# Kernel optimization log

Hardware: AMD Instinct MI355X
Metric: run time of the kernel (lower is better)

Reference implementation:

```python
import jax, jax.numpy as jnp
import numpy as np

N_EMBEDS = 1024
N_HEADS = 16
HEAD_DIM = N_EMBEDS // N_HEADS
SCALE = HEAD_DIM ** (-0.5)
B, T = 2, 2048


def setup_inputs() -> dict:
    key = jax.random.key(0)
    k1, k2, k3, k4 = jax.random.split(key, 4)
    x = jax.random.normal(k1, (B, T, N_EMBEDS), dtype=jnp.float32)
    # Glorot-uniform-style init like keras Dense defaults (scale irrelevant for correctness)
    w_qkv = jax.random.normal(k2, (N_EMBEDS, 3 * N_EMBEDS), dtype=jnp.float32) * (N_EMBEDS ** -0.5)
    w_proj = jax.random.normal(k3, (N_EMBEDS, N_EMBEDS), dtype=jnp.float32) * (N_EMBEDS ** -0.5)
    b_proj = jnp.zeros((N_EMBEDS,), dtype=jnp.float32)
    return {"x": x, "w_qkv": w_qkv, "w_proj": w_proj, "b_proj": b_proj}


def reference(x, w_qkv, w_proj, b_proj):
    Bc, Tc, D = x.shape
    qkv = x @ w_qkv                                   # [B,T,3D]
    q, k, v = jnp.split(qkv, 3, axis=-1)
    def heads(t):
        return t.reshape(Bc, Tc, N_HEADS, HEAD_DIM).transpose(0, 2, 1, 3)  # [B,H,T,hd]
    q, k, v = heads(q), heads(k), heads(v)
    att = jnp.einsum("bhqd,bhkd->bhqk", q, k) * SCALE  # [B,H,T,T]
    causal = jnp.tril(jnp.ones((Tc, Tc), dtype=bool))[None, None]
    att = jnp.where(causal, att, jnp.float32(-1e9))
    att = jax.nn.softmax(att, axis=-1)
    out = jnp.einsum("bhqk,bhkd->bhqd", att, v)        # [B,H,T,hd]
    out = out.transpose(0, 2, 1, 3).reshape(Bc, Tc, D)
    return out @ w_proj + b_proj
```

## Files before the change

kernel.cpp:

```cpp
#include <hip/hip_runtime.h>
#include <hip/hip_bf16.h>


typedef __bf16 bf16;
typedef float f32x4 __attribute__((ext_vector_type(4)));
typedef float f32x16 __attribute__((ext_vector_type(16)));
typedef bf16 bf16x4 __attribute__((ext_vector_type(4)));
typedef bf16 bf16x8 __attribute__((ext_vector_type(8)));

#define B_ 2
#define T_ 2048
#define D_ 1024
#define H_ 16
#define HD_ 64
#define QSPLIT 9

__device__ __forceinline__ f32x16 mfma32(bf16x8 a, bf16x8 b, f32x16 c) {
    return __builtin_amdgcn_mfma_f32_32x32x16_bf16(a, b, c, 0, 0, 0);
}

__device__ __forceinline__ void gload16(void* l, const void* g) {
    __builtin_amdgcn_global_load_lds(
        (const __attribute__((address_space(1))) unsigned int*)g,
        (__attribute__((address_space(3))) unsigned int*)l, 16, 0, 0);
}

__device__ __forceinline__ f32x16 z16() {
    f32x16 v;
#pragma unroll
    for (int i = 0; i < 16; ++i) v[i] = 0.f;
    return v;
}

__global__ __launch_bounds__(256) void prep(
    const float* __restrict__ x, bf16* __restrict__ xb,
    const float* __restrict__ wqkv, bf16* __restrict__ wqkvt,
    const float* __restrict__ wproj, bf16* __restrict__ wprojt) {
    __shared__ float tile[32][33];
    const int bid = blockIdx.x;
    const int tid = threadIdx.x;
    if (bid < 4096) {
        int i = bid * 256 + tid;
        float4 v = ((const float4*)x)[i];
        bf16x4 o = { (bf16)v.x, (bf16)v.y, (bf16)v.z, (bf16)v.w };
        ((bf16x4*)xb)[i] = o;
        return;
    }
    const float* in;
    bf16* outp;
    int C, bx, by;
    if (bid < 4096 + 3072) {
        int r = bid - 4096;
        in = wqkv; outp = wqkvt; C = 3 * D_; bx = r % 96; by = r / 96;
    } else {
        int r = bid - 7168;
        in = wproj; outp = wprojt; C = D_; bx = r % 32; by = r / 32;
    }
    const int R = D_;
    const int tx = tid & 31, ty = tid >> 5;
    int cx = bx * 32 + tx;
    int r0 = by * 32;
#pragma unroll
    for (int j = 0; j < 32; j += 8)
        tile[ty + j][tx] = in[(size_t)(r0 + ty + j) * C + cx];
    __syncthreads();
    int rx = r0 + tx;
    int c0 = bx * 32;
#pragma unroll
    for (int j = 0; j < 32; j += 8)
        outp[(size_t)(c0 + ty + j) * R + rx] = (bf16)tile[tx][ty + j];
}

template <int MW, int NWN, int EPI>
__global__ __launch_bounds__(256) void gemm_k(
    const bf16* __restrict__ A, const bf16* __restrict__ Bt,
    int M, int N, int K,
    bf16* __restrict__ qb, bf16* __restrict__ kb, bf16* __restrict__ vt,
    const float* __restrict__ bias, float* __restrict__ outf) {
    constexpr int BM = 64 * MW;
    constexpr int BN = 64 * NWN;
    __shared__ bf16 sA[BM * 64];
    __shared__ bf16 sB[BN * 64];
    const int tid = threadIdx.x;
    const int wave = tid >> 6, lane = tid & 63;
    const int ln = lane & 31, hi = lane >> 5;
    const int wr = (wave >> 1) * (32 * MW);
    const int wc = (wave & 1) * (32 * NWN);
    const int m0 = blockIdx.x * BM, n0 = blockIdx.y * BN;

    f32x16 acc[MW][NWN];
#pragma unroll
    for (int mi = 0; mi < MW; ++mi)
#pragma unroll
        for (int ni = 0; ni < NWN; ++ni) acc[mi][ni] = z16();

    for (int k0 = 0; k0 < K; k0 += 64) {
        __syncthreads();
#pragma unroll
        for (int j = 0; j < 2 * MW; ++j) {
            int c = tid + 256 * j;
            int r = c >> 3, g = (c & 7) ^ (r & 7);
            gload16(&sA[c * 8], A + (size_t)(m0 + r) * K + k0 + 8 * g);
        }
#pragma unroll
        for (int j = 0; j < 2 * NWN; ++j) {
            int c = tid + 256 * j;
            int r = c >> 3, g = (c & 7) ^ (r & 7);
            gload16(&sB[c * 8], Bt + (size_t)(n0 + r) * K + k0 + 8 * g);
        }
        __syncthreads();
#pragma unroll
        for (int s = 0; s < 4; ++s) {
            bf16x8 av[MW], bv[NWN];
#pragma unroll
            for (int mi = 0; mi < MW; ++mi) {
                int r = wr + mi * 32 + ln;
                av[mi] = *(const bf16x8*)((const char*)sA + r * 128 +
                                          ((((s << 1) | hi) ^ (r & 7)) << 4));
            }
#pragma unroll
            for (int ni = 0; ni < NWN; ++ni) {
                int r = wc + ni * 32 + ln;
                bv[ni] = *(const bf16x8*)((const char*)sB + r * 128 +
                                          ((((s << 1) | hi) ^ (r & 7)) << 4));
            }
#pragma unroll
            for (int mi = 0; mi < MW; ++mi)
#pragma unroll
                for (int ni = 0; ni < NWN; ++ni)
                    acc[mi][ni] = mfma32(av[mi], bv[ni], acc[mi][ni]);
        }
    }

#pragma unroll
    for (int mi = 0; mi < MW; ++mi)
#pragma unroll
        for (int ni = 0; ni < NWN; ++ni) {
            int col = n0 + wc + ni * 32 + ln;
            if (EPI == 0) {
                int part = col >> 10, h = (col >> 6) & 15, d = col & 63;
                if (part == 2) {
#pragma unroll
                    for (int g4 = 0; g4 < 4; ++g4) {
                        int row = m0 + wr + mi * 32 + 8 * g4 + 4 * hi;
                        int bb = row >> 11, tt = row & (T_ - 1);
                        bf16x4 w;
#pragma unroll
                        for (int j = 0; j < 4; ++j)
                            w[j] = (bf16)acc[mi][ni][4 * g4 + j];
                        *(bf16x4*)&vt[(((size_t)(bb * H_ + h) * HD_) + d) * T_ + tt] = w;
                    }
                } else {
                    bf16* dst = (part == 0) ? qb : kb;
                    float sc = (part == 0) ? 0.1803368801f : 1.0f;
#pragma unroll
                    for (int r = 0; r < 16; ++r) {
                        int row = m0 + wr + mi * 32 + (r & 3) + 8 * (r >> 2) + 4 * hi;
                        int bb = row >> 11, tt = row & (T_ - 1);
                        dst[((size_t)(bb * H_ + h) * T_ + tt) * HD_ + d] =
                            (bf16)(acc[mi][ni][r] * sc);
                    }
                }
            } else {
#pragma unroll
                for (int r = 0; r < 16; ++r) {
                    int row = m0 + wr + mi * 32 + (r & 3) + 8 * (r >> 2) + 4 * hi;
                    outf[(size_t)row * N + col] = acc[mi][ni][r] + bias[col];
                }
            }
        }
}

static __device__ const signed char QT_T[23] = {
    8, 7, 15, 15, 14, 14, 6, 13, 10, 10, 5, 11, 11, 12, 12, 13,
    0, 1, 2, 3, 4, 9, 9};
static __device__ const signed char SEG_T[23] = {
    -1, -1, 0, 1, 0, 1, -1, 0, 0, 1, -1, 0, 1, 0, 1, 1,
    -1, -1, -1, -1, -1, 0, 1};

__device__ __forceinline__ bf16x8 kread(const char* base, int row, int s, int hi) {
    int b = (row * 128 + s * 32 + hi * 16) ^ ((row & 7) << 4);
    return *(const bf16x8*)(base + b);
}
__device__ __forceinline__ bf16x8 vread(const char* base, int row, int s, int hi) {
    int sw = (row & 7) << 4;
    int b0 = (row * 128 + s * 32 + hi * 8) ^ sw;
    int b1 = (row * 128 + s * 32 + hi * 8 + 16) ^ sw;
    bf16x4 lo = *(const bf16x4*)(base + b0);
    bf16x4 hi4 = *(const bf16x4*)(base + b1);
    return __builtin_shufflevector(lo, hi4, 0, 1, 2, 3, 4, 5, 6, 7);
}

__global__ __launch_bounds__(256, 3) void attn_kernel(
    const bf16* __restrict__ qb, const bf16* __restrict__ kb,
    const bf16* __restrict__ vtb, bf16* __restrict__ ob,
    bf16* __restrict__ oP, float2* __restrict__ mlP) {
    __shared__ bf16 sK2[2][4096];
    __shared__ bf16 sV2[2][4096];

    const int bid = blockIdx.x;
    const int bh = bid & 31;
    const int sid = bid >> 5;
    const int qt = QT_T[sid];
    const int seg = SEG_T[sid];
    int t0, t1;
    if (seg < 0)       { t0 = 0;      t1 = 2 * qt + 2; }
    else if (seg == 0) { t0 = 0;      t1 = qt + 1; }
    else               { t0 = qt + 1; t1 = 2 * qt + 2; }
    const int b = bh >> 4, h = bh & 15;
    const int tid = threadIdx.x, wave = tid >> 6, lane = tid & 63;
    const int ln = lane & 31, hi = lane >> 5;
    const int qs = qt * 128 + wave * 32;
    const int qrow = qs + ln;

    const bf16* Qg = qb + (size_t)bh * (T_ * HD_);
    const bf16* Kg = kb + (size_t)bh * (T_ * HD_);
    const bf16* Vtg = vtb + (size_t)bh * (HD_ * T_);

    bf16x8 qf[4];
#pragma unroll
    for (int s = 0; s < 4; ++s)
        qf[s] = *(const bf16x8*)&Qg[(size_t)qrow * HD_ + s * 16 + hi * 8];
    bf16x8 ones;
#pragma unroll
    for (int e = 0; e < 8; ++e) ones[e] = (bf16)1.0f;

    const int rr0 = tid >> 3;
    const int gg = ((tid & 7) ^ (rr0 & 7)) * 8;

    {
        int kv0 = t0 * 64;
        gload16(&sK2[0][tid * 8], Kg + (size_t)(kv0 + rr0) * HD_ + gg);
        gload16(&sK2[0][(tid + 256) * 8], Kg + (size_t)(kv0 + rr0 + 32) * HD_ + gg);
        gload16(&sV2[0][tid * 8], Vtg + (size_t)rr0 * T_ + kv0 + gg);
        gload16(&sV2[0][(tid + 256) * 8], Vtg + (size_t)(rr0 + 32) * T_ + kv0 + gg);
    }
    __syncthreads();

    const float NINF = -__builtin_inff();
    f32x16 oA = z16(), oB = z16();
    float mR = NINF, lR = 0.f;
    int cur = 0;

    for (int t = t0; t < t1; ++t) {
        if ((t + 1) < t1) {
            int kv0 = (t + 1) * 64;
            bf16* kd = sK2[cur ^ 1];
            bf16* vd = sV2[cur ^ 1];
            gload16(&kd[tid * 8], Kg + (size_t)(kv0 + rr0) * HD_ + gg);
            gload16(&kd[(tid + 256) * 8], Kg + (size_t)(kv0 + rr0 + 32) * HD_ + gg);
            gload16(&vd[tid * 8], Vtg + (size_t)rr0 * T_ + kv0 + gg);
            gload16(&vd[(tid + 256) * 8], Vtg + (size_t)(rr0 + 32) * T_ + kv0 + gg);
        }

        if (64 * t <= qs + 31) {
            const char* kbase = (const char*)sK2[cur];
            const char* vbase = (const char*)sV2[cur];

            f32x16 p0 = z16(), p1 = z16();
            __builtin_amdgcn_s_setprio(1);
#pragma unroll
            for (int s = 0; s < 4; ++s) {
                bf16x8 a0 = kread(kbase, ln, s, hi);
                bf16x8 a1 = kread(kbase, ln + 32, s, hi);
                p0 = mfma32(a0, qf[s], p0);
                p1 = mfma32(a1, qf[s], p1);
            }
            __builtin_amdgcn_s_setprio(0);

            if (64 * t + 63 > qs) {
                int kvb = 64 * t + 4 * hi;
#pragma unroll
                for (int r = 0; r < 16; ++r) {
                    int kvr = kvb + (r & 3) + 8 * (r >> 2);
                    if (kvr > qrow) p0[r] = NINF;
                    if (kvr + 32 > qrow) p1[r] = NINF;
                }
            }

            float mx0 = NINF, mx1 = NINF, mx2 = NINF, mx3 = NINF;
#pragma unroll
            for (int r = 0; r < 16; r += 4) {
                mx0 = fmaxf(fmaxf(p0[r], p1[r]), mx0);
                mx1 = fmaxf(fmaxf(p0[r + 1], p1[r + 1]), mx1);
                mx2 = fmaxf(fmaxf(p0[r + 2], p1[r + 2]), mx2);
                mx3 = fmaxf(fmaxf(p0[r + 3], p1[r + 3]), mx3);
            }
            float pm = fmaxf(fmaxf(mx0, mx1), fmaxf(mx2, mx3));
            pm = fmaxf(pm, __shfl_xor(pm, 32));

            if (__any(pm > mR + 8.f)) {
                float mnew = fmaxf(mR, pm);
                float fac = exp2f(mR - mnew);
                lR *= fac;
#pragma unroll
                for (int r = 0; r < 16; ++r) { oA[r] *= fac; oB[r] *= fac; }
                mR = mnew;
            }

            bf16x8 pa0, pa1, pa2, pa3;
#pragma unroll
            for (int e = 0; e < 8; ++e) {
                pa0[e] = (bf16)exp2f(p0[e] - mR);
                pa1[e] = (bf16)exp2f(p0[8 + e] - mR);
                pa2[e] = (bf16)exp2f(p1[e] - mR);
                pa3[e] = (bf16)exp2f(p1[8 + e] - mR);
            }

            __builtin_amdgcn_s_setprio(1);
            f32x16 sacc = mfma32(ones, pa0, z16());
            sacc = mfma32(ones, pa1, sacc);
            sacc = mfma32(ones, pa2, sacc);
            sacc = mfma32(ones, pa3, sacc);
#pragma unroll
            for (int s = 0; s < 4; ++s) {
                bf16x8 pas = (s == 0) ? pa0 : (s == 1) ? pa1 : (s == 2) ? pa2 : pa3;
                oA = mfma32(vread(vbase, ln, s, hi), pas, oA);
                oB = mfma32(vread(vbase, ln + 32, s, hi), pas, oB);
            }
            __builtin_amdgcn_s_setprio(0);
            lR += sacc[0];
        }

        __syncthreads();
        cur ^= 1;
    }

    if (seg < 0) {
        float inv = 1.f / lR;
        bf16* orow = ob + ((size_t)(b * T_ + qrow)) * D_ + h * HD_;
#pragma unroll
        for (int g = 0; g < 4; ++g) {
            bf16x4 w, w2;
#pragma unroll
            for (int j = 0; j < 4; ++j) {
                w[j] = (bf16)(oA[4 * g + j] * inv);
                w2[j] = (bf16)(oB[4 * g + j] * inv);
            }
            *(bf16x4*)&orow[4 * hi + 8 * g] = w;
            *(bf16x4*)&orow[32 + 4 * hi + 8 * g] = w2;
        }
    } else {
        int row = wave * 32 + ln;
        bf16* prow;
        if (seg == 0) {
            prow = ob + ((size_t)(b * T_ + qrow)) * D_ + h * HD_;
        } else {
            size_t sbase = (size_t)bh * (16 - QSPLIT) + (qt - QSPLIT);
            prow = oP + (sbase * 128 + row) * 64;
        }
#pragma unroll
        for (int g = 0; g < 4; ++g) {
            bf16x4 w, w2;
#pragma unroll
            for (int j = 0; j < 4; ++j) {
                w[j] = (bf16)oA[4 * g + j];
                w2[j] = (bf16)oB[4 * g + j];
            }
            *(bf16x4*)&prow[4 * hi + 8 * g] = w;
            *(bf16x4*)&prow[32 + 4 * hi + 8 * g] = w2;
        }
        if (hi == 0)
            mlP[(((size_t)bh * (16 - QSPLIT) + (qt - QSPLIT)) * 2 + seg) * 128 + row] =
                make_float2(mR, lR);
    }
}

__global__ __launch_bounds__(256) void attn_merge(
    const bf16* __restrict__ oP, const float2* __restrict__ mlP,
    bf16* __restrict__ ob) {
    constexpr int NQS = 16 - QSPLIT;
    int gid = blockIdx.x * 256 + threadIdx.x;
    int bh = gid / (NQS * 128);
    int rem = gid - bh * (NQS * 128);
    int qi = rem >> 7, row = rem & 127;
    int b = bh >> 4, h = bh & 15;
    int t = (QSPLIT + qi) * 128 + row;
    size_t sbase = (size_t)bh * NQS + qi;
    float2 ml0 = mlP[(sbase * 2 + 0) * 128 + row];
    float2 ml1 = mlP[(sbase * 2 + 1) * 128 + row];
    float ms = fmaxf(ml0.x, ml1.x);
    float w0 = exp2f(ml0.x - ms), w1 = exp2f(ml1.x - ms);
    float inv = 1.f / (ml0.y * w0 + ml1.y * w1);
    w0 *= inv; w1 *= inv;
    bf16* dst = ob + ((size_t)(b * T_ + t)) * D_ + h * HD_;
    const bf16* r1 = oP + (sbase * 128 + row) * 64;
#pragma unroll
    for (int g = 0; g < 8; ++g) {
        bf16x8 a = *(const bf16x8*)&dst[g * 8];
        bf16x8 c = *(const bf16x8*)&r1[g * 8];
        bf16x8 o;
#pragma unroll
        for (int j = 0; j < 8; ++j)
            o[j] = (bf16)((float)a[j] * w0 + (float)c[j] * w1);
        *(bf16x8*)&dst[g * 8] = o;
    }
}

extern "C" void kernel_launch(void* const* d_in, const int* in_sizes, int n_in,
                              void* d_out, int out_size, void* d_ws, size_t ws_size,
                              hipStream_t stream) {
    const float* x = (const float*)d_in[0];
    const float* w_qkv = (const float*)d_in[1];
    const float* w_proj = (const float*)d_in[2];
    const float* b_proj = (const float*)d_in[3];
    float* out = (float*)d_out;
    char* ws = (char*)d_ws;

    bf16* xb = (bf16*)(ws);
    bf16* ob = (bf16*)(ws);
    bf16* wqkvt = (bf16*)(ws + 8388608);
    bf16* oP = (bf16*)(ws + 8388608);
    float2* mlP = (float2*)(ws + 12058624);
    bf16* wprojt = (bf16*)(ws + 14680064);
    bf16* qbuf = (bf16*)(ws + 16777216);
    bf16* kbuf = (bf16*)(ws + 25165824);
    bf16* vtbuf = (bf16*)(ws + 33554432);

    prep<<<8192, 256, 0, stream>>>(x, xb, w_qkv, wqkvt, w_proj, wprojt);

    gemm_k<2, 2, 0><<<dim3((B_ * T_) / 128, (3 * D_) / 128), 256, 0, stream>>>(
        xb, wqkvt, B_ * T_, 3 * D_, D_, qbuf, kbuf, vtbuf, nullptr, nullptr);

    attn_kernel<<<23 * 32, 256, 0, stream>>>(qbuf, kbuf, vtbuf, ob, oP, mlP);
    attn_merge<<<112, 256, 0, stream>>>(oP, mlP, ob);

    gemm_k<1, 2, 1><<<dim3((B_ * T_) / 64, D_ / 128), 256, 0, stream>>>(
        ob, wprojt, B_ * T_, D_, D_, nullptr, nullptr, nullptr, b_proj, out);
}
```

Before: 110.9 us.

## Fuse split-KV merge into attention kernel via per-strip atomic ticket

Removes the separate attn_merge launch. Each split attention block writes its partial output and its (m, l) statistics, then takes an atomic ticket on a per-strip counter. The second block to finish does the merge in registers, reading the other half from ob or oP. The counters live in the tail of the output buffer and are zeroed by the QKV GEMM. This saves one kernel launch and one pass over the partial data, at the cost of threadfences, an atomic and a dependency on workspace reuse.

New measurement: 204.8 us. 1.85x slower.

```diff
diff --git a/kernel.cpp b/kernel.cpp
--- a/kernel.cpp
+++ b/kernel.cpp
@@ -76,6 +76,7 @@
     const bf16* __restrict__ A, const bf16* __restrict__ Bt,
     int M, int N, int K,
     bf16* __restrict__ qb, bf16* __restrict__ kb, bf16* __restrict__ vt,
+    unsigned int* __restrict__ tick,
     const float* __restrict__ bias, float* __restrict__ outf) {
     constexpr int BM = 64 * MW;
     constexpr int BN = 64 * NWN;
@@ -88,6 +89,9 @@
     const int wc = (wave & 1) * (32 * NWN);
     const int m0 = blockIdx.x * BM, n0 = blockIdx.y * BN;
 
+    if (EPI == 0 && blockIdx.x == 0 && blockIdx.y == 0 && tid < 7 * 32)
+        tick[tid] = 0u;
+
     f32x16 acc[MW][NWN];
 #pragma unroll
     for (int mi = 0; mi < MW; ++mi)
@@ -194,9 +198,11 @@
 __global__ __launch_bounds__(256, 3) void attn_kernel(
     const bf16* __restrict__ qb, const bf16* __restrict__ kb,
     const bf16* __restrict__ vtb, bf16* __restrict__ ob,
-    bf16* __restrict__ oP, float2* __restrict__ mlP) {
+    bf16* __restrict__ oP, float2* __restrict__ mlP,
+    unsigned int* __restrict__ tick) {
     __shared__ bf16 sK2[2][4096];
     __shared__ bf16 sV2[2][4096];
+    __shared__ int sWin;
 
     const int bid = blockIdx.x;
     const int bh = bid & 31;
@@ -326,9 +332,11 @@
         cur ^= 1;
     }
 
+    const int row = wave * 32 + ln;
+    bf16* orow = ob + ((size_t)(b * T_ + qrow)) * D_ + h * HD_;
+
     if (seg < 0) {
         float inv = 1.f / lR;
-        bf16* orow = ob + ((size_t)(b * T_ + qrow)) * D_ + h * HD_;
 #pragma unroll
         for (int g = 0; g < 4; ++g) {
             bf16x4 w, w2;
@@ -340,60 +348,53 @@
             *(bf16x4*)&orow[4 * hi + 8 * g] = w;
             *(bf16x4*)&orow[32 + 4 * hi + 8 * g] = w2;
         }
-    } else {
-        int row = wave * 32 + ln;
-        bf16* prow;
-        if (seg == 0) {
-            prow = ob + ((size_t)(b * T_ + qrow)) * D_ + h * HD_;
-        } else {
-            size_t sbase = (size_t)bh * (16 - QSPLIT) + (qt - QSPLIT);
-            prow = oP + (sbase * 128 + row) * 64;
-        }
-#pragma unroll
-        for (int g = 0; g < 4; ++g) {
-            bf16x4 w, w2;
-#pragma unroll
-            for (int j = 0; j < 4; ++j) {
-                w[j] = (bf16)oA[4 * g + j];
-                w2[j] = (bf16)oB[4 * g + j];
-            }
-            *(bf16x4*)&prow[4 * hi + 8 * g] = w;
-            *(bf16x4*)&prow[32 + 4 * hi + 8 * g] = w2;
-        }
-        if (hi == 0)
-            mlP[(((size_t)bh * (16 - QSPLIT) + (qt - QSPLIT)) * 2 + seg) * 128 + row] =
-                make_float2(mR, lR);
-    }
-}
-
-__global__ __launch_bounds__(256) void attn_merge(
-    const bf16* __restrict__ oP, const float2* __restrict__ mlP,
-    bf16* __restrict__ ob) {
-    constexpr int NQS = 16 - QSPLIT;
-    int gid = blockIdx.x * 256 + threadIdx.x;
-    int bh = gid / (NQS * 128);
-    int rem = gid - bh * (NQS * 128);
-    int qi = rem >> 7, row = rem & 127;
-    int b = bh >> 4, h = bh & 15;
-    int t = (QSPLIT + qi) * 128 + row;
-    size_t sbase = (size_t)bh * NQS + qi;
-    float2 ml0 = mlP[(sbase * 2 + 0) * 128 + row];
-    float2 ml1 = mlP[(sbase * 2 + 1) * 128 + row];
-    float ms = fmaxf(ml0.x, ml1.x);
-    float w0 = exp2f(ml0.x - ms), w1 = exp2f(ml1.x - ms);
-    float inv = 1.f / (ml0.y * w0 + ml1.y * w1);
-    w0 *= inv; w1 *= inv;
-    bf16* dst = ob + ((size_t)(b * T_ + t)) * D_ + h * HD_;
-    const bf16* r1 = oP + (sbase * 128 + row) * 64;
-#pragma unroll
-    for (int g = 0; g < 8; ++g) {
-        bf16x8 a = *(const bf16x8*)&dst[g * 8];
-        bf16x8 c = *(const bf16x8*)&r1[g * 8];
-        bf16x8 o;
-#pragma unroll
-        for (int j = 0; j < 8; ++j)
-            o[j] = (bf16)((float)a[j] * w0 + (float)c[j] * w1);
-        *(bf16x8*)&dst[g * 8] = o;
+        return;
+    }
+
+    const int strip = qt - QSPLIT;
+    const size_t sbase = (size_t)bh * 7 + strip;
+    bf16* prow = (seg == 0) ? orow : oP + (sbase * 128 + row) * 64;
+#pragma unroll
+    for (int g = 0; g < 4; ++g) {
+        bf16x4 w, w2;
+#pragma unroll
+        for (int j = 0; j < 4; ++j) {
+            w[j] = (bf16)oA[4 * g + j];
+            w2[j] = (bf16)oB[4 * g + j];
+        }
+        *(bf16x4*)&prow[4 * hi + 8 * g] = w;
+        *(bf16x4*)&prow[32 + 4 * hi + 8 * g] = w2;
+    }
+    if (hi == 0) mlP[(sbase * 2 + seg) * 128 + row] = make_float2(mR, lR);
+
+    __threadfence();
+    __syncthreads();
+    if (tid == 0) {
+        unsigned int old = atomicAdd(&tick[sbase], 1u);
+        sWin = (int)(old & 1u);
+    }
+    __syncthreads();
+    if (!sWin) return;
+    __threadfence();
+
+    float2 mlo = mlP[(sbase * 2 + (seg ^ 1)) * 128 + row];
+    float ms = fmaxf(mR, mlo.x);
+    float ww = exp2f(mR - ms), wl = exp2f(mlo.x - ms);
+    float inv = 1.f / (lR * ww + mlo.y * wl);
+    ww *= inv; wl *= inv;
+    const bf16* lrow = (seg == 1) ? orow : oP + (sbase * 128 + row) * 64;
+#pragma unroll
+    for (int g = 0; g < 4; ++g) {
+        bf16x4 lo = *(const bf16x4*)&lrow[4 * hi + 8 * g];
+        bf16x4 lo2 = *(const bf16x4*)&lrow[32 + 4 * hi + 8 * g];
+        bf16x4 w, w2;
+#pragma unroll
+        for (int j = 0; j < 4; ++j) {
+            w[j] = (bf16)(oA[4 * g + j] * ww + (float)lo[j] * wl);
+            w2[j] = (bf16)(oB[4 * g + j] * ww + (float)lo2[j] * wl);
+        }
+        *(bf16x4*)&orow[4 * hi + 8 * g] = w;
+        *(bf16x4*)&orow[32 + 4 * hi + 8 * g] = w2;
     }
 }
 
@@ -416,15 +417,15 @@
     bf16* qbuf = (bf16*)(ws + 16777216);
     bf16* kbuf = (bf16*)(ws + 25165824);
     bf16* vtbuf = (bf16*)(ws + 33554432);
+    unsigned int* tick = (unsigned int*)(out + (size_t)B_ * T_ * D_ - 256);
 
     prep<<<8192, 256, 0, stream>>>(x, xb, w_qkv, wqkvt, w_proj, wprojt);
 
     gemm_k<2, 2, 0><<<dim3((B_ * T_) / 128, (3 * D_) / 128), 256, 0, stream>>>(
-        xb, wqkvt, B_ * T_, 3 * D_, D_, qbuf, kbuf, vtbuf, nullptr, nullptr);
-
-    attn_kernel<<<23 * 32, 256, 0, stream>>>(qbuf, kbuf, vtbuf, ob, oP, mlP);
-    attn_merge<<<112, 256, 0, stream>>>(oP, mlP, ob);
+        xb, wqkvt, B_ * T_, 3 * D_, D_, qbuf, kbuf, vtbuf, tick, nullptr, nullptr);
+
+    attn_kernel<<<23 * 32, 256, 0, stream>>>(qbuf, kbuf, vtbuf, ob, oP, mlP, tick);
 
     gemm_k<1, 2, 1><<<dim3((B_ * T_) / 64, D_ / 128), 256, 0, stream>>>(
-        ob, wprojt, B_ * T_, D_, D_, nullptr, nullptr, nullptr, b_proj, out);
-}
+        ob, wprojt, B_ * T_, D_, D_, nullptr, nullptr, nullptr, nullptr, b_proj, out);
+}
```
